# Kernel tuning notes

Measured on AMD Instinct MI355X. Metric: run time of the kernel, lower is better.

Reference implementation:

```python
import jax, jax.numpy as jnp
import numpy as np

H = 20   # num heads
D = 64   # head dim (hidden_size=1280)
N_IMG = 4
N_LBL = 4
SCALE_IMG = 1.0
SCALE_LBL = 1.0


def setup_inputs() -> dict:
    key = jax.random.key(0)
    ks = jax.random.split(key, 12)
    B, S, C, Dc = 4, 4096, 1280, 2048
    L = 77 + N_IMG + N_LBL  # 85 encoder tokens
    w = lambda k, shp: jax.random.normal(k, shp, dtype=jnp.float32) * 0.02
    return {
        "hidden_states": jax.random.normal(ks[0], (B, S, C), dtype=jnp.float32),
        "encoder_hidden_states": jax.random.normal(ks[1], (B, L, Dc), dtype=jnp.float32),
        "Wq": w(ks[2], (C, C)),
        "Wk": w(ks[3], (Dc, C)),
        "Wv": w(ks[4], (Dc, C)),
        "Wk_ip": w(ks[5], (Dc, C)),
        "Wv_ip": w(ks[6], (Dc, C)),
        "Wk_lbl": w(ks[7], (Dc, C)),
        "Wv_lbl": w(ks[8], (Dc, C)),
        "Wo": w(ks[9], (C, C)),
        "bo": jnp.zeros((C,), dtype=jnp.float32),
    }


def _attend(q, enc, Wk_, Wv_):
    # q: [B, S, H, D]; enc: [B, L, Dc]
    B, L = enc.shape[0], enc.shape[1]
    k = (enc @ Wk_).reshape(B, L, H, D)
    v = (enc @ Wv_).reshape(B, L, H, D)
    scores = jnp.einsum("bqhd,bkhd->bhqk", q, k) * (D ** -0.5)
    p = jax.nn.softmax(scores, axis=-1)
    return jnp.einsum("bhqk,bkhd->bqhd", p, v)


def reference(hidden_states, encoder_hidden_states, Wq, Wk, Wv,
              Wk_ip, Wv_ip, Wk_lbl, Wv_lbl, Wo, bo):
    B, S, C = hidden_states.shape
    end = encoder_hidden_states.shape[1] - N_IMG - N_LBL
    enc_text = encoder_hidden_states[:, :end]
    enc_img = encoder_hidden_states[:, end:end + N_IMG]
    enc_lbl = encoder_hidden_states[:, end + N_IMG:]

    q = (hidden_states @ Wq).reshape(B, S, H, D)

    out = _attend(q, enc_text, Wk, Wv)
    out = out + SCALE_IMG * _attend(q, enc_img, Wk_ip, Wv_ip)
    out = out + SCALE_LBL * _attend(q, enc_lbl, Wk_lbl, Wv_lbl)

    out = out.reshape(B, S, C) @ Wo + bo
    return out + hidden_states  # residual_connection=True, rescale=1.0
```

## Files before the change

kernel.cpp:

```cpp
#include <hip/hip_runtime.h>
#include <hip/hip_bf16.h>

typedef unsigned short u16;
using f32x4  = __attribute__((ext_vector_type(4))) float;
using bf16x8 = __attribute__((ext_vector_type(8))) short;

#define N_B 4
#define N_S 4096
#define N_C 1280
#define N_DC 2048
#define N_H 20
#define N_D 64

__device__ __forceinline__ u16 f2b(float f) {
  union { float f; unsigned u; } x; x.f = f;
  return (u16)((x.u + 0x7fffu + ((x.u >> 16) & 1u)) >> 16);
}

__device__ __forceinline__ void gld16(const u16* g, u16* l) {
  __builtin_amdgcn_global_load_lds(
      (const __attribute__((address_space(1))) unsigned int*)(g),
      (__attribute__((address_space(3))) unsigned int*)(l), 16, 0, 0);
}

struct TPargs { const float* s[8]; u16* d[8]; int K[8]; };

__global__ __launch_bounds__(256)
void k_prep(TPargs a, const float* __restrict__ hs, u16* __restrict__ hsb,
            const float* __restrict__ enc, u16* __restrict__ txt,
            u16* __restrict__ img, u16* __restrict__ lbl) {
  __shared__ float tl[64][65];
  int bx = blockIdx.x, t = threadIdx.x;
  if (bx < 5120) {
    int z = bx / 640, v = bx % 640;
    int n0 = (v % 20) * 64, k0 = (v / 20) * 64;
    int K = a.K[z];
    if (k0 >= K) return;
    const float* __restrict__ src = a.s[z];
    u16* __restrict__ dst = a.d[z];
    int r = t >> 4, c4 = (t & 15) * 4;
#pragma unroll
    for (int j = 0; j < 4; j++) {
      float4 v4 = *(const float4*)(src + (size_t)(k0 + j * 16 + r) * N_C + n0 + c4);
      tl[j * 16 + r][c4]     = v4.x;
      tl[j * 16 + r][c4 + 1] = v4.y;
      tl[j * 16 + r][c4 + 2] = v4.z;
      tl[j * 16 + r][c4 + 3] = v4.w;
    }
    __syncthreads();
    int n = t >> 3, koff = (t & 7) * 8;
#pragma unroll
    for (int j = 0; j < 2; j++) {
      int nn = j * 32 + n;
      alignas(16) u16 tmp[8];
#pragma unroll
      for (int kk = 0; kk < 8; kk++) tmp[kk] = f2b(tl[koff + kk][nn]);
      *(uint4*)(dst + (size_t)(n0 + nn) * K + k0 + koff) = *(uint4*)tmp;
    }
  } else if (bx < 7168) {
    int bv = bx - 5120;
    const int n8 = (N_B * N_S * N_C) / 8;
    for (int i = bv * 256 + t; i < n8; i += 2048 * 256) {
      const float4 v0 = *(const float4*)(hs + (size_t)i * 8);
      const float4 v1 = *(const float4*)(hs + (size_t)i * 8 + 4);
      alignas(16) u16 tmp[8];
      tmp[0] = f2b(v0.x); tmp[1] = f2b(v0.y); tmp[2] = f2b(v0.z); tmp[3] = f2b(v0.w);
      tmp[4] = f2b(v1.x); tmp[5] = f2b(v1.y); tmp[6] = f2b(v1.z); tmp[7] = f2b(v1.w);
      *(uint4*)(hsb + (size_t)i * 8) = *(uint4*)tmp;
    }
  } else {
    int row = bx - 7168;
    int b = row / 85, l = row % 85;
    const float* s = enc + (size_t)row * N_DC;
    u16* d;
    if (l < 77)      d = txt + (size_t)(b * 77 + l) * N_DC;
    else if (l < 81) d = img + (size_t)(b * 4 + (l - 77)) * N_DC;
    else             d = lbl + (size_t)(b * 4 + (l - 81)) * N_DC;
    for (int i = t * 8; i < N_DC; i += 256 * 8) {
      const float4 v0 = *(const float4*)(s + i);
      const float4 v1 = *(const float4*)(s + i + 4);
      alignas(16) u16 tmp[8];
      tmp[0] = f2b(v0.x); tmp[1] = f2b(v0.y); tmp[2] = f2b(v0.z); tmp[3] = f2b(v0.w);
      tmp[4] = f2b(v1.x); tmp[5] = f2b(v1.y); tmp[6] = f2b(v1.z); tmp[7] = f2b(v1.w);
      *(uint4*)(d + i) = *(uint4*)tmp;
    }
  }
}

__device__ __forceinline__ void stage32(const u16* __restrict__ g, int ldK,
                                        int row0, int kk, u16* ldsb,
                                        int w, int lane) {
  int r = row0 + w * 8 + (lane >> 3);
  int gslot = ((lane & 7) ^ (lane >> 3)) << 3;
  gld16(g + (size_t)r * ldK + kk + gslot, ldsb + w * 512);
}
__device__ __forceinline__ void stageA(const u16* Ag, int K, int kk, u16* ldsb,
                                       int w, int lane) {
#pragma unroll
  for (int j = 0; j < 4; j++)
    stage32(Ag, K, j * 32, kk, ldsb + j * 2048, w, lane);
}
__device__ __forceinline__ void stageB(const u16* Bg, int K, int kk, u16* ldsb,
                                       int w, int lane) {
#pragma unroll
  for (int j = 0; j < 5; j++)
    stage32(Bg, K, j * 32, kk, ldsb + j * 2048, w, lane);
}

#define RD_A2(aoff, mh)                                                      \
  _Pragma("unroll") for (int mi = 0; mi < 2; mi++) {                         \
    _Pragma("unroll") for (int ks = 0; ks < 2; ks++) {                       \
      int row = wr * 64 + ((mh) * 2 + mi) * 16 + lrow;                       \
      int slot = (ks * 4 + g) ^ (lane & 7);                                  \
      af[mi][ks] = *(const bf16x8*)&lds[(aoff) + row * 64 + slot * 8];       \
    }                                                                        \
  }

#define RD_B5(boff)                                                          \
  _Pragma("unroll") for (int n = 0; n < 5; n++) {                            \
    _Pragma("unroll") for (int ks = 0; ks < 2; ks++) {                       \
      int row = wc * 80 + n * 16 + lrow;                                     \
      int slot = (ks * 4 + g) ^ (lane & 7);                                  \
      bf[n][ks] = *(const bf16x8*)&lds[(boff) + row * 64 + slot * 8];        \
    }                                                                        \
  }

#define MFMA10(mh)                                                           \
  _Pragma("unroll") for (int ks = 0; ks < 2; ks++) {                         \
    _Pragma("unroll") for (int n = 0; n < 5; n++)                            \
      acc[mh][n] = __builtin_amdgcn_mfma_f32_16x16x32_bf16(                  \
          af[(mh) & 1][ks], bf[n][ks], acc[mh][n], 0, 0, 0);                 \
  }

#define BARR()  __builtin_amdgcn_s_barrier()
#define VM0()   asm volatile("s_waitcnt vmcnt(0)" ::: "memory")
#define PRIO(x) __builtin_amdgcn_s_setprio(x)

template<int EPI>
__device__ __forceinline__ void gemm_body(
    const u16* __restrict__ A, const u16* __restrict__ Bt, void* __restrict__ Cv,
    int M, int N, int K, float scale,
    const float* __restrict__ bias, const float* __restrict__ resid,
    u16* lds, int bid, int nwg) {
  const int t = threadIdx.x, lane = t & 63, w = t >> 6;
  const int wr = w >> 1, wc = w & 1;
  const int lrow = lane & 15, g = lane >> 4;

  int nt = N / 160;
  int swz = ((nwg & 7) == 0) ? ((bid & 7) * (nwg >> 3) + (bid >> 3)) : bid;
  int bm = swz / nt, bn = swz % nt;

  const u16* Ag = A  + (size_t)bm * 128 * K;
  const u16* Bg = Bt + (size_t)bn * 160 * K;
  const int NT = K >> 6;

  f32x4 acc[4][5] = {};
  bf16x8 af[2][2], bf[5][2];

  stageA(Ag, K, 0, lds + 0,     w, lane);
  stageB(Bg, K, 0, lds + 16384, w, lane);
  VM0();
  BARR();

  for (int tt = 0; tt < NT; ++tt) {
    int c = tt & 1;
    int aof  = c * 8192,        bof  = 16384 + c * 10240;
    int aof1 = (c ^ 1) * 8192,  bof1 = 16384 + (c ^ 1) * 10240;
    if (tt + 1 < NT) {
      stageA(Ag, K, (tt + 1) * 64, lds + aof1, w, lane);
      stageB(Bg, K, (tt + 1) * 64, lds + bof1, w, lane);
    }
    RD_B5(bof);
    RD_A2(aof, 0);
    PRIO(1); MFMA10(0); MFMA10(1); PRIO(0);
    RD_A2(aof, 1);
    PRIO(1); MFMA10(2); MFMA10(3); PRIO(0);
    VM0();
    BARR();
  }

#pragma unroll
  for (int m = 0; m < 4; m++) {
    int row = bm * 128 + wr * 64 + m * 16 + g * 4;
#pragma unroll
    for (int n = 0; n < 5; n++) {
      int col = bn * 160 + wc * 80 + n * 16 + lrow;
#pragma unroll
      for (int j = 0; j < 4; j++) {
        float v = acc[m][n][j];
        if constexpr (EPI == 1)
          ((u16*)Cv)[(size_t)(row + j) * N + col] = f2b(v * scale);
        else
          ((float*)Cv)[(size_t)(row + j) * N + col] =
              v + bias[col] + resid[(size_t)(row + j) * N + col];
      }
    }
  }
}

__device__ __forceinline__ void kv_body(
    const u16* __restrict__ A, const u16* __restrict__ Bt, u16* __restrict__ C,
    int M, int bm, int bn, u16* ldsraw) {
  u16 (*lds)[2][8192] = (u16(*)[2][8192])ldsraw;
  const int K = 2048;
  int t = threadIdx.x, lane = t & 63, w = t >> 6;
  int wm = w >> 1, wn = w & 1;
  int c8 = lane & 7, rsub = lane >> 3;

  f32x4 acc[4][4] = {};

#define KVSTAGE(kt, buf)                                                      \
  {                                                                           \
    int k0 = (kt) * 64;                                                       \
    _Pragma("unroll") for (int i2 = 0; i2 < 4; i2++) {                        \
      int rloc = w * 32 + i2 * 8;                                             \
      int ra = bm * 128 + rloc + rsub; if (ra >= M) ra = M - 1;               \
      int rb = bn * 128 + rloc + rsub;                                        \
      gld16(A  + (size_t)ra * K + k0 + c8 * 8, &lds[buf][0][rloc * 64]);      \
      gld16(Bt + (size_t)rb * K + k0 + c8 * 8, &lds[buf][1][rloc * 64]);      \
    }                                                                         \
  }

  KVSTAGE(0, 0);
  VM0();
  __syncthreads();
  int cur = 0;
  for (int kt = 0; kt < 32; kt++) {
    if (kt < 31) KVSTAGE(kt + 1, cur ^ 1);
#pragma unroll
    for (int ks = 0; ks < 2; ks++) {
      bf16x8 afr[4], bfr[4];
#pragma unroll
      for (int m = 0; m < 4; m++)
        afr[m] = *(bf16x8*)&lds[cur][0][(wm * 64 + m * 16 + (lane & 15)) * 64 + ks * 32 + (lane >> 4) * 8];
#pragma unroll
      for (int n = 0; n < 4; n++)
        bfr[n] = *(bf16x8*)&lds[cur][1][(wn * 64 + n * 16 + (lane & 15)) * 64 + ks * 32 + (lane >> 4) * 8];
#pragma unroll
      for (int m = 0; m < 4; m++)
#pragma unroll
        for (int n = 0; n < 4; n++)
          acc[m][n] = __builtin_amdgcn_mfma_f32_16x16x32_bf16(afr[m], bfr[n], acc[m][n], 0, 0, 0);
    }
    VM0();
    __syncthreads();
    cur ^= 1;
  }
#undef KVSTAGE

#pragma unroll
  for (int m = 0; m < 4; m++) {
    int row = bm * 128 + wm * 64 + m * 16 + ((lane >> 4) << 2);
#pragma unroll
    for (int n = 0; n < 4; n++) {
      int col = bn * 128 + wn * 64 + n * 16 + (lane & 15);
#pragma unroll
      for (int j = 0; j < 4; j++) {
        int r = row + j;
        if (r >= M) continue;
        C[(size_t)r * 1280 + col] = f2b(acc[m][n][j]);
      }
    }
  }
}

__global__ __launch_bounds__(256, 2)
void qkv_gemm(const u16* __restrict__ hsb, const u16* __restrict__ wq,
              u16* __restrict__ qbuf,
              const u16* __restrict__ etxt, const u16* __restrict__ eimg,
              const u16* __restrict__ elbl,
              const u16* __restrict__ wk,   const u16* __restrict__ wv,
              const u16* __restrict__ wkip, const u16* __restrict__ wvip,
              const u16* __restrict__ wklb, const u16* __restrict__ wvlb,
              u16* ktxt, u16* vtxt, u16* kimg, u16* vimg, u16* klbl, u16* vlbl) {
  __shared__ __align__(16) u16 lds[36864];
  int bx = blockIdx.x;
  if (bx < 100) {
    int bn = bx % 10, my = (bx / 10) % 5, kv = bx / 50;
    const u16 *A, *Bt; u16* C; int M, bm;
    if (my < 3)       { A = etxt; M = 308; bm = my; Bt = kv ? wv   : wk;   C = kv ? vtxt : ktxt; }
    else if (my == 3) { A = eimg; M = 16;  bm = 0;  Bt = kv ? wvip : wkip; C = kv ? vimg : kimg; }
    else              { A = elbl; M = 16;  bm = 0;  Bt = kv ? wvlb : wklb; C = kv ? vlbl : klbl; }
    kv_body(A, Bt, C, M, bm, bn, lds);
  } else {
    gemm_body<1>(hsb, wq, qbuf, 16384, 1280, 1280, 0.125f, nullptr, nullptr,
                 lds, bx - 100, 1024);
  }
}

__global__ __launch_bounds__(256, 2)
void gemm_o(const u16* __restrict__ A, const u16* __restrict__ Bt,
            float* __restrict__ Cv, const float* __restrict__ bias,
            const float* __restrict__ resid) {
  __shared__ __align__(16) u16 lds[36864];
  gemm_body<2>(A, Bt, Cv, 16384, 1280, 1280, 1.f, bias, resid,
               lds, blockIdx.x, 1024);
}

#define QSTR 72
#define PSTR 104

__global__ __launch_bounds__(256, 2)
void attn_kern(const u16* __restrict__ q,
               const u16* __restrict__ ktxt, const u16* __restrict__ vtxt,
               const u16* __restrict__ kimg, const u16* __restrict__ vimg,
               const u16* __restrict__ klbl, const u16* __restrict__ vlbl,
               u16* __restrict__ outa) {
  __shared__ __align__(16) char smem[45568];
  u16* Qs = (u16*)smem;
  u16* Ks = (u16*)(smem + 18432);
  u16* Ps = (u16*)smem;
  u16* Vt = (u16*)(smem + 32256);

  int st = blockIdx.x, h = blockIdx.y, b = blockIdx.z;
  int t = threadIdx.x, lane = t & 63, w = t >> 6;
  int s0 = st * 128;
  int c = lane & 15, g = lane >> 4;

  for (int i = t; i < 27136 / 16; i += 256)
    ((uint4*)(smem + 18432))[i] = make_uint4(0, 0, 0, 0);
#pragma unroll
  for (int i = 0; i < 4; i++) {
    int cid = t + i * 256; int r = cid >> 3, c8 = cid & 7;
    *(uint4*)&Qs[r * QSTR + c8 * 8] =
        *(const uint4*)(q + (size_t)(b * N_S + s0 + r) * N_C + h * N_D + c8 * 8);
  }
  __syncthreads();
  for (int cid = t; cid < 680; cid += 256) {
    int l = cid >> 3, c8 = cid & 7;
    const u16* p;
    if (l < 77)      p = ktxt + (size_t)(b * 77 + l) * N_C + h * N_D + c8 * 8;
    else if (l < 81) p = kimg + (size_t)(b * 4 + l - 77) * N_C + h * N_D + c8 * 8;
    else             p = klbl + (size_t)(b * 4 + l - 81) * N_C + h * N_D + c8 * 8;
    int row = (l < 77) ? l : l + 3;
    *(uint4*)&Ks[row * QSTR + c8 * 8] = *(const uint4*)p;
  }
  for (int e = t; e < 85 * 64; e += 256) {
    int l = e >> 6, d = e & 63;
    const u16* p;
    if (l < 77)      p = vtxt + (size_t)(b * 77 + l) * N_C + h * N_D + d;
    else if (l < 81) p = vimg + (size_t)(b * 4 + l - 77) * N_C + h * N_D + d;
    else             p = vlbl + (size_t)(b * 4 + l - 81) * N_C + h * N_D + d;
    int slot = (l < 77) ? l : l + 3;
    Vt[d * PSTR + slot] = *p;
  }
  __syncthreads();

  f32x4 sacc[2][6] = {};
#pragma unroll
  for (int ks = 0; ks < 2; ks++) {
    bf16x8 aq[2], bk[6];
#pragma unroll
    for (int m = 0; m < 2; m++)
      aq[m] = *(bf16x8*)&Qs[(w * 32 + m * 16 + c) * QSTR + ks * 32 + g * 8];
#pragma unroll
    for (int n = 0; n < 6; n++)
      bk[n] = *(bf16x8*)&Ks[(n * 16 + c) * QSTR + ks * 32 + g * 8];
#pragma unroll
    for (int m = 0; m < 2; m++)
#pragma unroll
      for (int n = 0; n < 6; n++)
        sacc[m][n] = __builtin_amdgcn_mfma_f32_16x16x32_bf16(aq[m], bk[n], sacc[m][n], 0, 0, 0);
  }
  __syncthreads();

  const float NEG = -1e30f;
#pragma unroll
  for (int m = 0; m < 2; m++) {
#pragma unroll
    for (int j = 0; j < 4; j++) {
      float tmax = NEG;
#pragma unroll
      for (int n = 0; n < 5; n++)
        if (n * 16 + c < 77) tmax = fmaxf(tmax, sacc[m][n][j]);
#pragma unroll
      for (int off = 1; off < 16; off <<= 1) tmax = fmaxf(tmax, __shfl_xor(tmax, off));
      float pv[5], tsum = 0.f;
#pragma unroll
      for (int n = 0; n < 5; n++) {
        float v = (n * 16 + c < 77) ? __expf(sacc[m][n][j] - tmax) : 0.f;
        pv[n] = v; tsum += v;
      }
#pragma unroll
      for (int off = 1; off < 16; off <<= 1) tsum += __shfl_xor(tsum, off);
      float v5 = sacc[m][5][j];
      float imax = (c < 4) ? v5 : NEG;
#pragma unroll
      for (int off = 1; off < 16; off <<= 1) imax = fmaxf(imax, __shfl_xor(imax, off));
      float ie = (c < 4) ? __expf(v5 - imax) : 0.f, isum = ie;
#pragma unroll
      for (int off = 1; off < 16; off <<= 1) isum += __shfl_xor(isum, off);
      float lmax = (c >= 4 && c < 8) ? v5 : NEG;
#pragma unroll
      for (int off = 1; off < 16; off <<= 1) lmax = fmaxf(lmax, __shfl_xor(lmax, off));
      float le = (c >= 4 && c < 8) ? __expf(v5 - lmax) : 0.f, lsum = le;
#pragma unroll
      for (int off = 1; off < 16; off <<= 1) lsum += __shfl_xor(lsum, off);

      float rt = 1.f / tsum;
      float p5 = (c < 4) ? ie / isum : ((c < 8) ? le / lsum : 0.f);
      int rowl = w * 32 + m * 16 + g * 4 + j;
#pragma unroll
      for (int n = 0; n < 5; n++)
        Ps[rowl * PSTR + n * 16 + c] = f2b(pv[n] * rt);
      Ps[rowl * PSTR + 80 + c] = f2b(p5);
    }
  }
  __syncthreads();

  f32x4 oacc[2][4] = {};
#pragma unroll
  for (int ks = 0; ks < 3; ks++) {
    bf16x8 ap[2], bv[4];
#pragma unroll
    for (int m = 0; m < 2; m++)
      ap[m] = *(bf16x8*)&Ps[(w * 32 + m * 16 + c) * PSTR + ks * 32 + g * 8];
#pragma unroll
    for (int n = 0; n < 4; n++)
      bv[n] = *(bf16x8*)&Vt[(n * 16 + c) * PSTR + ks * 32 + g * 8];
#pragma unroll
    for (int m = 0; m < 2; m++)
#pragma unroll
      for (int n = 0; n < 4; n++)
        oacc[m][n] = __builtin_amdgcn_mfma_f32_16x16x32_bf16(ap[m], bv[n], oacc[m][n], 0, 0, 0);
  }

#pragma unroll
  for (int m = 0; m < 2; m++) {
    int rbase = w * 32 + m * 16 + g * 4;
#pragma unroll
    for (int n = 0; n < 4; n++) {
      int d = n * 16 + c;
#pragma unroll
      for (int j = 0; j < 4; j++) {
        int s = s0 + rbase + j;
        outa[(size_t)(b * N_S + s) * N_C + h * N_D + d] = f2b(oacc[m][n][j]);
      }
    }
  }
}

extern "C" void kernel_launch(void* const* d_in, const int* in_sizes, int n_in,
                              void* d_out, int out_size, void* d_ws, size_t ws_size,
                              hipStream_t stream) {
  const float* hs   = (const float*)d_in[0];
  const float* enc  = (const float*)d_in[1];
  const float* Wq   = (const float*)d_in[2];
  const float* Wk   = (const float*)d_in[3];
  const float* Wv   = (const float*)d_in[4];
  const float* Wkip = (const float*)d_in[5];
  const float* Wvip = (const float*)d_in[6];
  const float* Wklb = (const float*)d_in[7];
  const float* Wvlb = (const float*)d_in[8];
  const float* Wo   = (const float*)d_in[9];
  const float* bo   = (const float*)d_in[10];

  if (ws_size < 83087360u) return;
  char* ws = (char*)d_ws;
  u16* wq_t   = (u16*)(ws + 0);
  u16* wo_t   = (u16*)(ws + 3276800);
  u16* wk_t   = (u16*)(ws + 6553600);
  u16* wv_t   = (u16*)(ws + 11796480);
  u16* wkip_t = (u16*)(ws + 17039360);
  u16* wvip_t = (u16*)(ws + 22282240);
  u16* wklb_t = (u16*)(ws + 27525120);
  u16* wvlb_t = (u16*)(ws + 32768000);
  u16* etxt   = (u16*)(ws + 38010880);
  u16* eimg   = (u16*)(ws + 39272448);
  u16* elbl   = (u16*)(ws + 39337984);
  u16* ktxt   = (u16*)(ws + 39403520);
  u16* vtxt   = (u16*)(ws + 40192000);
  u16* kimg   = (u16*)(ws + 40980480);
  u16* vimg   = (u16*)(ws + 41021440);
  u16* klbl   = (u16*)(ws + 41062400);
  u16* vlbl   = (u16*)(ws + 41103360);
  u16* attn   = (u16*)(ws + 41144320);
  u16* qbuf   = (u16*)d_out;
  u16* hsb    = (u16*)d_out + (size_t)N_S * N_B * N_C;

  TPargs tp;
  tp.s[0] = Wq;   tp.d[0] = wq_t;   tp.K[0] = 1280;
  tp.s[1] = Wo;   tp.d[1] = wo_t;   tp.K[1] = 1280;
  tp.s[2] = Wk;   tp.d[2] = wk_t;   tp.K[2] = 2048;
  tp.s[3] = Wv;   tp.d[3] = wv_t;   tp.K[3] = 2048;
  tp.s[4] = Wkip; tp.d[4] = wkip_t; tp.K[4] = 2048;
  tp.s[5] = Wvip; tp.d[5] = wvip_t; tp.K[5] = 2048;
  tp.s[6] = Wklb; tp.d[6] = wklb_t; tp.K[6] = 2048;
  tp.s[7] = Wvlb; tp.d[7] = wvlb_t; tp.K[7] = 2048;

  k_prep<<<7508, 256, 0, stream>>>(tp, hs, hsb, enc, etxt, eimg, elbl);

  qkv_gemm<<<1124, 256, 0, stream>>>(hsb, wq_t, qbuf,
                                     etxt, eimg, elbl,
                                     wk_t, wv_t, wkip_t, wvip_t, wklb_t, wvlb_t,
                                     ktxt, vtxt, kimg, vimg, klbl, vlbl);

  attn_kern<<<dim3(32, N_H, N_B), 256, 0, stream>>>(qbuf, ktxt, vtxt, kimg, vimg,
                                                    klbl, vlbl, attn);
  gemm_o<<<1024, 256, 0, stream>>>(attn, wo_t, (float*)d_out, bo, hs);
}
```

Baseline: 225.7 us.

## Fuse hidden_states bf16 conversion into Q projection GEMM A-tile loads

Drops the separate pass that converts hidden_states from fp32 to bf16 in the prep kernel. The Q GEMM now loads fp32 A tiles into registers, converts them to bf16 and writes them into swizzled LDS after the MFMA phase, in place of the async global_load_lds staging. This removes a full write and re-read of the 16384x1280 bf16 activation copy. In exchange the Q GEMM reads twice the A bytes, holds more registers for the prefetched tiles, and adds conversion ALU work and LDS writes inside the main loop.

```diff
diff --git a/kernel.cpp b/kernel.cpp
--- a/kernel.cpp
+++ b/kernel.cpp
@@ -26,8 +26,7 @@
 struct TPargs { const float* s[8]; u16* d[8]; int K[8]; };
 
 __global__ __launch_bounds__(256)
-void k_prep(TPargs a, const float* __restrict__ hs, u16* __restrict__ hsb,
-            const float* __restrict__ enc, u16* __restrict__ txt,
+void k_prep(TPargs a, const float* __restrict__ enc, u16* __restrict__ txt,
             u16* __restrict__ img, u16* __restrict__ lbl) {
   __shared__ float tl[64][65];
   int bx = blockIdx.x, t = threadIdx.x;
@@ -57,19 +56,8 @@
       for (int kk = 0; kk < 8; kk++) tmp[kk] = f2b(tl[koff + kk][nn]);
       *(uint4*)(dst + (size_t)(n0 + nn) * K + k0 + koff) = *(uint4*)tmp;
     }
-  } else if (bx < 7168) {
-    int bv = bx - 5120;
-    const int n8 = (N_B * N_S * N_C) / 8;
-    for (int i = bv * 256 + t; i < n8; i += 2048 * 256) {
-      const float4 v0 = *(const float4*)(hs + (size_t)i * 8);
-      const float4 v1 = *(const float4*)(hs + (size_t)i * 8 + 4);
-      alignas(16) u16 tmp[8];
-      tmp[0] = f2b(v0.x); tmp[1] = f2b(v0.y); tmp[2] = f2b(v0.z); tmp[3] = f2b(v0.w);
-      tmp[4] = f2b(v1.x); tmp[5] = f2b(v1.y); tmp[6] = f2b(v1.z); tmp[7] = f2b(v1.w);
-      *(uint4*)(hsb + (size_t)i * 8) = *(uint4*)tmp;
-    }
   } else {
-    int row = bx - 7168;
+    int row = bx - 5120;
     int b = row / 85, l = row % 85;
     const float* s = enc + (size_t)row * N_DC;
     u16* d;
@@ -106,6 +94,22 @@
   for (int j = 0; j < 5; j++)
     stage32(Bg, K, j * 32, kk, ldsb + j * 2048, w, lane);
 }
+__device__ __forceinline__ void ldA_f32(const float* __restrict__ Af, int K,
+                                        int row0, int kk, int w, int lane,
+                                        float4& lo, float4& hi) {
+  int r = row0 + w * 8 + (lane >> 3);
+  int gs = ((lane & 7) ^ (lane >> 3)) << 3;
+  const float* p = Af + (size_t)r * K + kk + gs;
+  lo = *(const float4*)p;
+  hi = *(const float4*)(p + 4);
+}
+__device__ __forceinline__ void wrA_bf16(u16* ldsb, int w, int lane,
+                                         float4 lo, float4 hi) {
+  alignas(16) u16 tmp[8];
+  tmp[0] = f2b(lo.x); tmp[1] = f2b(lo.y); tmp[2] = f2b(lo.z); tmp[3] = f2b(lo.w);
+  tmp[4] = f2b(hi.x); tmp[5] = f2b(hi.y); tmp[6] = f2b(hi.z); tmp[7] = f2b(hi.w);
+  *(uint4*)&ldsb[w * 512 + lane * 8] = *(uint4*)tmp;
+}
 
 #define RD_A2(aoff, mh)                                                      \
   _Pragma("unroll") for (int mi = 0; mi < 2; mi++) {                         \
@@ -134,11 +138,12 @@
 
 #define BARR()  __builtin_amdgcn_s_barrier()
 #define VM0()   asm volatile("s_waitcnt vmcnt(0)" ::: "memory")
+#define LGKM0() asm volatile("s_waitcnt lgkmcnt(0)" ::: "memory")
 #define PRIO(x) __builtin_amdgcn_s_setprio(x)
 
-template<int EPI>
+template<int EPI, int AF32>
 __device__ __forceinline__ void gemm_body(
-    const u16* __restrict__ A, const u16* __restrict__ Bt, void* __restrict__ Cv,
+    const void* __restrict__ Av, const u16* __restrict__ Bt, void* __restrict__ Cv,
     int M, int N, int K, float scale,
     const float* __restrict__ bias, const float* __restrict__ resid,
     u16* lds, int bid, int nwg) {
@@ -150,15 +155,26 @@
   int swz = ((nwg & 7) == 0) ? ((bid & 7) * (nwg >> 3) + (bid >> 3)) : bid;
   int bm = swz / nt, bn = swz % nt;
 
-  const u16* Ag = A  + (size_t)bm * 128 * K;
-  const u16* Bg = Bt + (size_t)bn * 160 * K;
+  const u16*   Ab = (const u16*)Av   + (size_t)bm * 128 * K;
+  const float* Af = (const float*)Av + (size_t)bm * 128 * K;
+  const u16*   Bg = Bt + (size_t)bn * 160 * K;
   const int NT = K >> 6;
 
   f32x4 acc[4][5] = {};
   bf16x8 af[2][2], bf[5][2];
 
-  stageA(Ag, K, 0, lds + 0,     w, lane);
+  if constexpr (AF32) {
+#pragma unroll
+    for (int j = 0; j < 4; j++) {
+      float4 lo, hi;
+      ldA_f32(Af, K, j * 32, 0, w, lane, lo, hi);
+      wrA_bf16(lds + j * 2048, w, lane, lo, hi);
+    }
+  } else {
+    stageA(Ab, K, 0, lds + 0, w, lane);
+  }
   stageB(Bg, K, 0, lds + 16384, w, lane);
+  LGKM0();
   VM0();
   BARR();
 
@@ -166,15 +182,32 @@
     int c = tt & 1;
     int aof  = c * 8192,        bof  = 16384 + c * 10240;
     int aof1 = (c ^ 1) * 8192,  bof1 = 16384 + (c ^ 1) * 10240;
-    if (tt + 1 < NT) {
-      stageA(Ag, K, (tt + 1) * 64, lds + aof1, w, lane);
-      stageB(Bg, K, (tt + 1) * 64, lds + bof1, w, lane);
+    bool st = (tt + 1 < NT);
+    int kn = st ? (tt + 1) * 64 : 0;
+    float4 lo[4], hi[4];
+    if (st) {
+      if constexpr (AF32) {
+#pragma unroll
+        for (int j = 0; j < 4; j++)
+          ldA_f32(Af, K, j * 32, kn, w, lane, lo[j], hi[j]);
+      } else {
+        stageA(Ab, K, kn, lds + aof1, w, lane);
+      }
+      stageB(Bg, K, kn, lds + bof1, w, lane);
     }
     RD_B5(bof);
     RD_A2(aof, 0);
     PRIO(1); MFMA10(0); MFMA10(1); PRIO(0);
     RD_A2(aof, 1);
     PRIO(1); MFMA10(2); MFMA10(3); PRIO(0);
+    if (st) {
+      if constexpr (AF32) {
+#pragma unroll
+        for (int j = 0; j < 4; j++)
+          wrA_bf16(lds + aof1 + j * 2048, w, lane, lo[j], hi[j]);
+        LGKM0();
+      }
+    }
     VM0();
     BARR();
   }
@@ -265,7 +298,7 @@
 }
 
 __global__ __launch_bounds__(256, 2)
-void qkv_gemm(const u16* __restrict__ hsb, const u16* __restrict__ wq,
+void qkv_gemm(const float* __restrict__ hs, const u16* __restrict__ wq,
               u16* __restrict__ qbuf,
               const u16* __restrict__ etxt, const u16* __restrict__ eimg,
               const u16* __restrict__ elbl,
@@ -283,8 +316,8 @@
     else              { A = elbl; M = 16;  bm = 0;  Bt = kv ? wvlb : wklb; C = kv ? vlbl : klbl; }
     kv_body(A, Bt, C, M, bm, bn, lds);
   } else {
-    gemm_body<1>(hsb, wq, qbuf, 16384, 1280, 1280, 0.125f, nullptr, nullptr,
-                 lds, bx - 100, 1024);
+    gemm_body<1, 1>(hs, wq, qbuf, 16384, 1280, 1280, 0.125f, nullptr, nullptr,
+                    lds, bx - 100, 1024);
   }
 }
 
@@ -293,8 +326,8 @@
             float* __restrict__ Cv, const float* __restrict__ bias,
             const float* __restrict__ resid) {
   __shared__ __align__(16) u16 lds[36864];
-  gemm_body<2>(A, Bt, Cv, 16384, 1280, 1280, 1.f, bias, resid,
-               lds, blockIdx.x, 1024);
+  gemm_body<2, 0>(A, Bt, Cv, 16384, 1280, 1280, 1.f, bias, resid,
+                  lds, blockIdx.x, 1024);
 }
 
 #define QSTR 72
@@ -476,7 +509,6 @@
   u16* vlbl   = (u16*)(ws + 41103360);
   u16* attn   = (u16*)(ws + 41144320);
   u16* qbuf   = (u16*)d_out;
-  u16* hsb    = (u16*)d_out + (size_t)N_S * N_B * N_C;
 
   TPargs tp;
   tp.s[0] = Wq;   tp.d[0] = wq_t;   tp.K[0] = 1280;
@@ -488,9 +520,9 @@
   tp.s[6] = Wklb; tp.d[6] = wklb_t; tp.K[6] = 2048;
   tp.s[7] = Wvlb; tp.d[7] = wvlb_t; tp.K[7] = 2048;
 
-  k_prep<<<7508, 256, 0, stream>>>(tp, hs, hsb, enc, etxt, eimg, elbl);
-
-  qkv_gemm<<<1124, 256, 0, stream>>>(hsb, wq_t, qbuf,
+  k_prep<<<5460, 256, 0, stream>>>(tp, enc, etxt, eimg, elbl);
+
+  qkv_gemm<<<1124, 256, 0, stream>>>(hs, wq_t, qbuf,
                                      etxt, eimg, elbl,
                                      wk_t, wv_t, wkip_t, wvip_t, wklb_t, wvlb_t,
                                      ktxt, vtxt, kimg, vimg, klbl, vlbl);
```

Result: slower. 247.6 us (+9.7%).

## Move Wo transpose into attention launch and swizzle KV GEMM LDS layout

Applied to the files above, without the earlier changes.

Takes the Wo weight transpose/convert out of the prep kernel and runs it as 400 extra blocks appended to the attention kernel grid, now flattened to 1D, so that work overlaps with attention instead of lengthening the prep stage. It also applies an XOR swizzle to the LDS staging layout in the KV projection GEMM, both on the global-to-LDS writes and the fragment reads, to cut LDS bank conflicts. The cost is extra branching in the attention kernel and a small transpose workload competing with attention blocks for compute units.

```diff
diff --git a/kernel.cpp b/kernel.cpp
--- a/kernel.cpp
+++ b/kernel.cpp
@@ -25,40 +25,45 @@
 
 struct TPargs { const float* s[8]; u16* d[8]; int K[8]; };
 
+__device__ __forceinline__ void tp_tile(const float* __restrict__ src,
+                                        u16* __restrict__ dst, int K,
+                                        int n0, int k0, int t, char* smem) {
+  float (*tl)[65] = (float(*)[65])smem;
+  int r = t >> 4, c4 = (t & 15) * 4;
+#pragma unroll
+  for (int j = 0; j < 4; j++) {
+    float4 v4 = *(const float4*)(src + (size_t)(k0 + j * 16 + r) * N_C + n0 + c4);
+    tl[j * 16 + r][c4]     = v4.x;
+    tl[j * 16 + r][c4 + 1] = v4.y;
+    tl[j * 16 + r][c4 + 2] = v4.z;
+    tl[j * 16 + r][c4 + 3] = v4.w;
+  }
+  __syncthreads();
+  int n = t >> 3, koff = (t & 7) * 8;
+#pragma unroll
+  for (int j = 0; j < 2; j++) {
+    int nn = j * 32 + n;
+    alignas(16) u16 tmp[8];
+#pragma unroll
+    for (int kk = 0; kk < 8; kk++) tmp[kk] = f2b(tl[koff + kk][nn]);
+    *(uint4*)(dst + (size_t)(n0 + nn) * K + k0 + koff) = *(uint4*)tmp;
+  }
+}
+
 __global__ __launch_bounds__(256)
 void k_prep(TPargs a, const float* __restrict__ hs, u16* __restrict__ hsb,
             const float* __restrict__ enc, u16* __restrict__ txt,
             u16* __restrict__ img, u16* __restrict__ lbl) {
-  __shared__ float tl[64][65];
+  __shared__ __align__(16) char smem[16640];
   int bx = blockIdx.x, t = threadIdx.x;
-  if (bx < 5120) {
+  if (bx < 4480) {
     int z = bx / 640, v = bx % 640;
     int n0 = (v % 20) * 64, k0 = (v / 20) * 64;
     int K = a.K[z];
     if (k0 >= K) return;
-    const float* __restrict__ src = a.s[z];
-    u16* __restrict__ dst = a.d[z];
-    int r = t >> 4, c4 = (t & 15) * 4;
-#pragma unroll
-    for (int j = 0; j < 4; j++) {
-      float4 v4 = *(const float4*)(src + (size_t)(k0 + j * 16 + r) * N_C + n0 + c4);
-      tl[j * 16 + r][c4]     = v4.x;
-      tl[j * 16 + r][c4 + 1] = v4.y;
-      tl[j * 16 + r][c4 + 2] = v4.z;
-      tl[j * 16 + r][c4 + 3] = v4.w;
-    }
-    __syncthreads();
-    int n = t >> 3, koff = (t & 7) * 8;
-#pragma unroll
-    for (int j = 0; j < 2; j++) {
-      int nn = j * 32 + n;
-      alignas(16) u16 tmp[8];
-#pragma unroll
-      for (int kk = 0; kk < 8; kk++) tmp[kk] = f2b(tl[koff + kk][nn]);
-      *(uint4*)(dst + (size_t)(n0 + nn) * K + k0 + koff) = *(uint4*)tmp;
-    }
-  } else if (bx < 7168) {
-    int bv = bx - 5120;
+    tp_tile(a.s[z], a.d[z], K, n0, k0, t, smem);
+  } else if (bx < 6528) {
+    int bv = bx - 4480;
     const int n8 = (N_B * N_S * N_C) / 8;
     for (int i = bv * 256 + t; i < n8; i += 2048 * 256) {
       const float4 v0 = *(const float4*)(hs + (size_t)i * 8);
@@ -69,7 +74,7 @@
       *(uint4*)(hsb + (size_t)i * 8) = *(uint4*)tmp;
     }
   } else {
-    int row = bx - 7168;
+    int row = bx - 6528;
     int b = row / 85, l = row % 85;
     const float* s = enc + (size_t)row * N_DC;
     u16* d;
@@ -205,7 +210,8 @@
   const int K = 2048;
   int t = threadIdx.x, lane = t & 63, w = t >> 6;
   int wm = w >> 1, wn = w & 1;
-  int c8 = lane & 7, rsub = lane >> 3;
+  int gs = ((lane & 7) ^ (lane >> 3)) * 8;
+  int rsub = lane >> 3;
 
   f32x4 acc[4][4] = {};
 
@@ -216,8 +222,8 @@
       int rloc = w * 32 + i2 * 8;                                             \
       int ra = bm * 128 + rloc + rsub; if (ra >= M) ra = M - 1;               \
       int rb = bn * 128 + rloc + rsub;                                        \
-      gld16(A  + (size_t)ra * K + k0 + c8 * 8, &lds[buf][0][rloc * 64]);      \
-      gld16(Bt + (size_t)rb * K + k0 + c8 * 8, &lds[buf][1][rloc * 64]);      \
+      gld16(A  + (size_t)ra * K + k0 + gs, &lds[buf][0][rloc * 64]);          \
+      gld16(Bt + (size_t)rb * K + k0 + gs, &lds[buf][1][rloc * 64]);          \
     }                                                                         \
   }
 
@@ -231,11 +237,17 @@
     for (int ks = 0; ks < 2; ks++) {
       bf16x8 afr[4], bfr[4];
 #pragma unroll
-      for (int m = 0; m < 4; m++)
-        afr[m] = *(bf16x8*)&lds[cur][0][(wm * 64 + m * 16 + (lane & 15)) * 64 + ks * 32 + (lane >> 4) * 8];
-#pragma unroll
-      for (int n = 0; n < 4; n++)
-        bfr[n] = *(bf16x8*)&lds[cur][1][(wn * 64 + n * 16 + (lane & 15)) * 64 + ks * 32 + (lane >> 4) * 8];
+      for (int m = 0; m < 4; m++) {
+        int row = wm * 64 + m * 16 + (lane & 15);
+        int slot = (ks * 4 + (lane >> 4)) ^ (lane & 7);
+        afr[m] = *(bf16x8*)&lds[cur][0][row * 64 + slot * 8];
+      }
+#pragma unroll
+      for (int n = 0; n < 4; n++) {
+        int row = wn * 64 + n * 16 + (lane & 15);
+        int slot = (ks * 4 + (lane >> 4)) ^ (lane & 7);
+        bfr[n] = *(bf16x8*)&lds[cur][1][row * 64 + slot * 8];
+      }
 #pragma unroll
       for (int m = 0; m < 4; m++)
 #pragma unroll
@@ -305,15 +317,24 @@
                const u16* __restrict__ ktxt, const u16* __restrict__ vtxt,
                const u16* __restrict__ kimg, const u16* __restrict__ vimg,
                const u16* __restrict__ klbl, const u16* __restrict__ vlbl,
-               u16* __restrict__ outa) {
+               u16* __restrict__ outa,
+               const float* __restrict__ Wo, u16* __restrict__ wo_t) {
   __shared__ __align__(16) char smem[45568];
+  int bx = blockIdx.x;
+  int t = threadIdx.x;
+  if (bx >= 2560) {
+    int v = bx - 2560;
+    int n0 = (v % 20) * 64, k0 = (v / 20) * 64;
+    tp_tile(Wo, wo_t, 1280, n0, k0, t, smem);
+    return;
+  }
   u16* Qs = (u16*)smem;
   u16* Ks = (u16*)(smem + 18432);
   u16* Ps = (u16*)smem;
   u16* Vt = (u16*)(smem + 32256);
 
-  int st = blockIdx.x, h = blockIdx.y, b = blockIdx.z;
-  int t = threadIdx.x, lane = t & 63, w = t >> 6;
+  int st = bx & 31, h = (bx >> 5) % 20, b = bx / 640;
+  int lane = t & 63, w = t >> 6;
   int s0 = st * 128;
   int c = lane & 15, g = lane >> 4;
 
@@ -480,22 +501,23 @@
 
   TPargs tp;
   tp.s[0] = Wq;   tp.d[0] = wq_t;   tp.K[0] = 1280;
-  tp.s[1] = Wo;   tp.d[1] = wo_t;   tp.K[1] = 1280;
-  tp.s[2] = Wk;   tp.d[2] = wk_t;   tp.K[2] = 2048;
-  tp.s[3] = Wv;   tp.d[3] = wv_t;   tp.K[3] = 2048;
-  tp.s[4] = Wkip; tp.d[4] = wkip_t; tp.K[4] = 2048;
-  tp.s[5] = Wvip; tp.d[5] = wvip_t; tp.K[5] = 2048;
-  tp.s[6] = Wklb; tp.d[6] = wklb_t; tp.K[6] = 2048;
-  tp.s[7] = Wvlb; tp.d[7] = wvlb_t; tp.K[7] = 2048;
-
-  k_prep<<<7508, 256, 0, stream>>>(tp, hs, hsb, enc, etxt, eimg, elbl);
+  tp.s[1] = Wk;   tp.d[1] = wk_t;   tp.K[1] = 2048;
+  tp.s[2] = Wv;   tp.d[2] = wv_t;   tp.K[2] = 2048;
+  tp.s[3] = Wkip; tp.d[3] = wkip_t; tp.K[3] = 2048;
+  tp.s[4] = Wvip; tp.d[4] = wvip_t; tp.K[4] = 2048;
+  tp.s[5] = Wklb; tp.d[5] = wklb_t; tp.K[5] = 2048;
+  tp.s[6] = Wvlb; tp.d[6] = wvlb_t; tp.K[6] = 2048;
+  tp.s[7] = Wo;   tp.d[7] = wo_t;   tp.K[7] = 1280;
+
+  k_prep<<<6868, 256, 0, stream>>>(tp, hs, hsb, enc, etxt, eimg, elbl);
 
   qkv_gemm<<<1124, 256, 0, stream>>>(hsb, wq_t, qbuf,
                                      etxt, eimg, elbl,
                                      wk_t, wv_t, wkip_t, wvip_t, wklb_t, wvlb_t,
                                      ktxt, vtxt, kimg, vimg, klbl, vlbl);
 
-  attn_kern<<<dim3(32, N_H, N_B), 256, 0, stream>>>(qbuf, ktxt, vtxt, kimg, vimg,
-                                                    klbl, vlbl, attn);
+  attn_kern<<<2960, 256, 0, stream>>>(qbuf, ktxt, vtxt, kimg, vimg,
+                                      klbl, vlbl, attn, Wo, wo_t);
+
   gemm_o<<<1024, 256, 0, stream>>>(attn, wo_t, (float*)d_out, bo, hs);
 }
```

Result: no change. 229.2 us (+1.6%).
